# Optimization experiments

Hardware: AMD Instinct MI355X
Metric: run time of the kernel (lower is better)

The kernel has to match this reference:

```python
import jax, jax.numpy as jnp
import numpy as np

H, W, C = 128, 128, 100
N_OBJ = 3
PAD_VAL = 1e20  # WRONG_LABEL_PADDING-style padding used by local_pairwise_distances2


def setup_inputs() -> dict:
    key = jax.random.key(0)
    k1, k2, k3 = jax.random.split(key, 3)
    return {
        "prev_frame_embedding": jax.random.normal(k1, (H, W, C), dtype=jnp.float32),
        "query_embedding": jax.random.normal(k2, (H, W, C), dtype=jnp.float32),
        "prev_frame_labels": jax.random.randint(k3, (H, W, 1), 0, N_OBJ),
        "gt_ids": jnp.arange(N_OBJ),
        "max_distance": 15,
    }


def _local_nn_features(query_embedding, prev_frame_embedding, prev_frame_labels, gt_ids, max_distance):
    h, w, c = query_embedding.shape
    k = 2 * max_distance + 1  # static python int -> static shapes
    n_obj = gt_ids.shape[0]

    # masks: [h, w, n_obj] -- labels are [h, w, 1], broadcast against gt_ids
    masks = prev_frame_labels == gt_ids[None, None, :]

    # pad reference embedding with a huge value (matches torch F.pad value=1e20),
    # pad masks with False (matches torch zero padding)
    y_pad = jnp.pad(prev_frame_embedding,
                    ((max_distance, max_distance), (max_distance, max_distance), (0, 0)),
                    constant_values=PAD_VAL)
    m_pad = jnp.pad(masks,
                    ((max_distance, max_distance), (max_distance, max_distance), (0, 0)))

    # offsets in the same order as the torch nested loops (y_start outer, x_start inner)
    offs = jnp.stack(jnp.meshgrid(jnp.arange(k), jnp.arange(k), indexing="ij"), -1).reshape(-1, 2)

    x = query_embedding

    def per_offset(off):
        y_sl = jax.lax.dynamic_slice(y_pad, (off[0], off[1], 0), (h, w, c))
        m_sl = jax.lax.dynamic_slice(m_pad, (off[0], off[1], 0), (h, w, n_obj))
        diff = x - y_sl
        d = jnp.sum(diff * diff, axis=-1)  # [h, w]
        return d, m_sl

    # sequential map over the k*k window offsets keeps peak memory small
    d, offset_masks = jax.lax.map(per_offset, offs)  # [k2,h,w], [k2,h,w,n_obj]
    d = jnp.transpose(d, (1, 2, 0))                   # [h, w, k2]
    offset_masks = jnp.transpose(offset_masks, (1, 2, 0, 3))  # [h, w, k2, n_obj]

    # mask out wrong-object / out-of-frame offsets with distance 1.0 (torch pad=ones_like)
    d_masked = jnp.where(offset_masks, d[..., None], jnp.float32(1.0))
    dists = jnp.min(d_masked, axis=2)  # [h, w, n_obj]
    return dists.reshape(1, h, w, n_obj, 1)


def reference(prev_frame_embedding, query_embedding, prev_frame_labels, gt_ids, max_distance):
    return _local_nn_features(query_embedding, prev_frame_embedding,
                              prev_frame_labels, gt_ids, max_distance)
```

## Files before the change

### kernel.cpp

```cpp
#include <hip/hip_runtime.h>
#include <cstdint>


#define HW   128
#define NC   100
#define MD   15
#define NOBJ 3
#define PIX  (HW * HW)
#define NOUT (PIX * NOBJ)
#define PEN_NM (1 << 22)
#define CSENT  (1 << 28)
#define IINIT  (1 << 30)

typedef __attribute__((ext_vector_type(4))) int intx4;

__device__ inline intx4 quant_pack16(const float* v) {
    signed char b[16];
#pragma unroll
    for (int j = 0; j < 16; ++j) {
        int qi = __float2int_rn(v[j] * 32.f);
        b[j] = (signed char)max(-127, min(127, qi));
    }
    intx4 r;
#pragma unroll
    for (int w = 0; w < 4; ++w)
        r[w] = (b[4*w] & 255) | ((b[4*w+1] & 255) << 8) |
               ((b[4*w+2] & 255) << 16) | ((b[4*w+3] & 255) << 24);
    return r;
}

__global__ __launch_bounds__(256) void vos_prep(
    const float* __restrict__ P, const float* __restrict__ Q,
    const int* __restrict__ labels,
    signed char* __restrict__ Pq, signed char* __restrict__ Qa,
    int2* __restrict__ yl, float* __restrict__ x2)
{
    const int lane = threadIdx.x & 63;
    const int wid  = blockIdx.x * 4 + (threadIdx.x >> 6);

    if (wid < 2048) {
        const int pix = wid * 8 + (lane >> 3);
        const int col = pix & 127;
        const int c = lane & 7;
        const float* sp = P + (size_t)pix * NC;
        const int k0 = c * 16;
        float v[16];
#pragma unroll
        for (int c4 = 0; c4 < 4; ++c4) {
            float4 a = {0.f,0.f,0.f,0.f};
            if (k0 + c4 * 4 + 4 <= NC) a = *(const float4*)(sp + k0 + c4 * 4);
            v[c4*4+0]=a.x; v[c4*4+1]=a.y; v[c4*4+2]=a.z; v[c4*4+3]=a.w;
        }
        *(intx4*)(Pq + (size_t)pix * 128 + ((c ^ (col & 7)) << 4)) = quant_pack16(v);
        float part = 0.f;
#pragma unroll
        for (int j = 0; j < 16; ++j) part = fmaf(v[j], v[j], part);
        part += __shfl_xor(part, 1); part += __shfl_xor(part, 2); part += __shfl_xor(part, 4);
        if ((lane & 7) == 0)
            yl[pix] = make_int2(__float2int_rn(part * 512.f), labels[pix]);
    } else if (wid < 4096) {
        const int w2 = wid - 2048;
        const int row = w2 >> 4, rem = w2 & 15;
        const int tile = rem >> 1, kh = rem & 1;
        const int m = lane & 15, quad = lane >> 4;
        const int pix = row * HW + tile * 16 + m;
        const float* sp = Q + (size_t)pix * NC;
        const int k0 = kh * 64 + quad * 16;
        float v[16];
#pragma unroll
        for (int c4 = 0; c4 < 4; ++c4) {
            float4 a = {0.f,0.f,0.f,0.f};
            if (k0 + c4 * 4 + 4 <= NC) a = *(const float4*)(sp + k0 + c4 * 4);
            v[c4*4+0]=a.x; v[c4*4+1]=a.y; v[c4*4+2]=a.z; v[c4*4+3]=a.w;
        }
        *(intx4*)(Qa + ((size_t)((row*8 + tile)*2 + kh))*1024 + lane*16) = quant_pack16(v);
    } else {
        const int w3 = wid - 4096;
        const int pix = w3 * 8 + (lane >> 3);
        const int lp = lane & 7;
        const float* sp = Q + (size_t)pix * NC;
        float part = 0.f;
#pragma unroll
        for (int cc = 0; cc < 4; ++cc) {
            int k = lp * 16 + cc * 4;
            if (k <= 96) {
                float4 t = *(const float4*)(sp + k);
                part = fmaf(t.x,t.x,part); part = fmaf(t.y,t.y,part);
                part = fmaf(t.z,t.z,part); part = fmaf(t.w,t.w,part);
            }
        }
        part += __shfl_xor(part, 1); part += __shfl_xor(part, 2); part += __shfl_xor(part, 4);
        if (lp == 0) x2[pix] = part;
    }
}

__device__ inline void stage_row(const signed char* __restrict__ Pq,
                                 signed char* dst, int r, int wv, int lane) {
    const signed char* src = Pq + (size_t)r * 16384 + wv * 4096;
    signed char* d = dst + wv * 4096;
#pragma unroll
    for (int it = 0; it < 4; ++it)
        __builtin_amdgcn_global_load_lds(
            (const __attribute__((address_space(1))) unsigned int*)(src + it * 1024 + lane * 16),
            (__attribute__((address_space(3))) unsigned int*)(d + it * 1024), 16, 0, 0);
}

__global__ __launch_bounds__(256, 2) void vos_band(
    const signed char* __restrict__ Pq, const signed char* __restrict__ Qa,
    const int2* __restrict__ yl, const int* __restrict__ gt,
    float* __restrict__ part)
{
    __shared__ signed char Bs[2][2][16384];
    __shared__ int2 yl_s[4 * 128];

    const int tid  = threadIdx.x;
    const int lane = tid & 63;
    const int wv   = tid >> 6;
    const int quad = lane >> 4;
    const int n    = lane & 15;
    const int j0w  = wv * 32;

    const int b      = blockIdx.x;
    const int xcd    = b & 7;
    const int wi     = b >> 3;
    const int stripe = xcd * 8 + (wi & 7);
    const int ck     = wi >> 3;
    const int i0     = stripe * 2;
    const int rbase  = i0 - MD + ck * 4;
    const int rlo    = max(rbase, 0);
    const int rhi    = min(rbase + 4, HW);
    const int np     = (rhi > rlo) ? ((rhi - rlo + 1) >> 1) : 0;

    const int g0 = gt[0], g1 = gt[1], g2 = gt[2];

    if (np > 0) {
        stage_row(Pq, &Bs[0][0][0], rlo, wv, lane);
        if (rlo + 1 < rhi) stage_row(Pq, &Bs[0][1][0], rlo + 1, wv, lane);
    }

    for (int t = tid; t < 4 * 128; t += 256) {
        int rr = t >> 7, c = t & 127, r = rbase + rr;
        if ((unsigned)r < (unsigned)HW) yl_s[t] = yl[r * HW + c];
    }

    intx4 Af[2][2][2];
#pragma unroll
    for (int uc = 0; uc < 2; ++uc)
#pragma unroll
    for (int ur = 0; ur < 2; ++ur) {
        const signed char* bse = Qa + (size_t)((i0 + ur) * 8 + wv * 2 + uc) * 2048;
#pragma unroll
        for (int kh = 0; kh < 2; ++kh)
            Af[uc][ur][kh] = *(const intx4*)(bse + kh * 1024 + lane * 16);
    }

    bool bgt[4], blt[4];
#pragma unroll
    for (int reg = 0; reg < 4; ++reg) {
        int m = quad * 4 + reg;
        bgt[reg] = n > m;
        blt[reg] = n < m;
    }

    int mm[2][2][4][NOBJ];
#pragma unroll
    for (int uc = 0; uc < 2; ++uc)
#pragma unroll
    for (int ur = 0; ur < 2; ++ur)
#pragma unroll
    for (int reg = 0; reg < 4; ++reg) {
        mm[uc][ur][reg][0] = IINIT; mm[uc][ur][reg][1] = IINIT; mm[uc][ur][reg][2] = IINIT;
    }

    __syncthreads();

    for (int pi = 0; pi < np; ++pi) {
        const int ra = rlo + 2 * pi;
        const int rb = ra + 1;
        if (pi + 1 < np) {
            const int r2 = ra + 2;
            stage_row(Pq, &Bs[(pi + 1) & 1][0][0], r2, wv, lane);
            if (r2 + 1 < rhi) stage_row(Pq, &Bs[(pi + 1) & 1][1][0], r2 + 1, wv, lane);
        }

        const signed char* BA = &Bs[pi & 1][0][0];
        const signed char* BB = &Bs[pi & 1][1][0];
        const bool hasB = rb < rhi;
        bool rvA[2], rvB[2];
        rvA[0] = (unsigned)(ra - i0 + MD)     <= 2u * MD;
        rvA[1] = (unsigned)(ra - i0 - 1 + MD) <= 2u * MD;
        rvB[0] = hasB && ((unsigned)(rb - i0 + MD)     <= 2u * MD);
        rvB[1] = hasB && ((unsigned)(rb - i0 - 1 + MD) <= 2u * MD);
        const int rrA = (ra - rbase) * 128;
        const int rrB = (min(rb, rhi - 1) - rbase) * 128;

#pragma unroll
        for (int t = 0; t < 4; ++t) {
            const int base = j0w + 16 * (t - 1);
            if (base < 0 || base >= HW) continue;

            const int pcol = base + n;
            int2 ylA = yl_s[rrA + pcol];
            int2 ylB = yl_s[rrB + pcol];
            int pA0 = (ylA.y == g0) ? ylA.x : PEN_NM;
            int pA1 = (ylA.y == g1) ? ylA.x : PEN_NM;
            int pA2 = (ylA.y == g2) ? ylA.x : PEN_NM;
            int pB0 = (ylB.y == g0) ? ylB.x : PEN_NM;
            int pB1 = (ylB.y == g1) ? ylB.x : PEN_NM;
            int pB2 = (ylB.y == g2) ? ylB.x : PEN_NM;

            intx4 CA[2][2], CB[2][2];
#pragma unroll
            for (int uc = 0; uc < 2; ++uc)
#pragma unroll
            for (int ur = 0; ur < 2; ++ur) {
                CA[uc][ur] = (intx4){0,0,0,0};
                CB[uc][ur] = (intx4){0,0,0,0};
            }

#pragma unroll
            for (int kh = 0; kh < 2; ++kh) {
                const int off = pcol * 128 + (((kh * 4 + quad) ^ (pcol & 7)) << 4);
                intx4 bvA = *(const intx4*)(BA + off);
                intx4 bvB = *(const intx4*)(BB + off);
#pragma unroll
                for (int uc = 0; uc < 2; ++uc) {
                    if (uc == 0 && t == 3) continue;
                    if (uc == 1 && t == 0) continue;
#pragma unroll
                    for (int ur = 0; ur < 2; ++ur) {
                        CA[uc][ur] = __builtin_amdgcn_mfma_i32_16x16x64_i8(Af[uc][ur][kh], bvA, CA[uc][ur], 0, 0, 0);
                        CB[uc][ur] = __builtin_amdgcn_mfma_i32_16x16x64_i8(Af[uc][ur][kh], bvB, CB[uc][ur], 0, 0, 0);
                    }
                }
            }

#pragma unroll
            for (int uc = 0; uc < 2; ++uc) {
                if (uc == 0 && t == 3) continue;
                if (uc == 1 && t == 0) continue;
                const int du = t - 1 - uc;
#pragma unroll
                for (int ur = 0; ur < 2; ++ur) {
#pragma unroll
                    for (int reg = 0; reg < 4; ++reg) {
                        bool tri = (du == 0) | (du == -1 ? bgt[reg] : blt[reg]);
                        bool okA = rvA[ur] & tri;
                        bool okB = rvB[ur] & tri;
                        int cA = okA ? CA[uc][ur][reg] : -CSENT;
                        int cB = okB ? CB[uc][ur][reg] : -CSENT;
                        mm[uc][ur][reg][0] = min(min(mm[uc][ur][reg][0], pA0 - cA), pB0 - cB);
                        mm[uc][ur][reg][1] = min(min(mm[uc][ur][reg][1], pA1 - cA), pB1 - cB);
                        mm[uc][ur][reg][2] = min(min(mm[uc][ur][reg][2], pA2 - cA), pB2 - cB);
                    }
                }
            }
        }
        __syncthreads();
    }

#pragma unroll
    for (int s = 1; s < 16; s <<= 1) {
#pragma unroll
        for (int uc = 0; uc < 2; ++uc)
#pragma unroll
        for (int ur = 0; ur < 2; ++ur)
#pragma unroll
        for (int reg = 0; reg < 4; ++reg)
#pragma unroll
        for (int o = 0; o < NOBJ; ++o)
            mm[uc][ur][reg][o] = min(mm[uc][ur][reg][o], __shfl_xor(mm[uc][ur][reg][o], s));
    }

    float* ps = (float*)&Bs[0][0][0];
    if (n == 0) {
#pragma unroll
        for (int uc = 0; uc < 2; ++uc)
#pragma unroll
        for (int ur = 0; ur < 2; ++ur)
#pragma unroll
        for (int reg = 0; reg < 4; ++reg) {
            const int qcol = j0w + 16 * uc + quad * 4 + reg;
#pragma unroll
            for (int o = 0; o < NOBJ; ++o)
                ps[(ur * 128 + qcol) * 3 + o] = (float)mm[uc][ur][reg][o];
        }
    }
    __syncthreads();
    if (tid < 192) {
        float4 v = *(const float4*)(ps + tid * 4);
        *(float4*)(part + (size_t)ck * NOUT + i0 * 384 + tid * 4) = v;
    }
}

__global__ __launch_bounds__(256) void vos_combine(
    const float* __restrict__ part, const float* __restrict__ x2,
    float* __restrict__ out)
{
    const int t = blockIdx.x * 256 + threadIdx.x;
    float v = part[t];
#pragma unroll
    for (int ck = 1; ck < 8; ++ck) v = fminf(v, part[ck * NOUT + t]);
    v = v * (1.f / 512.f) + x2[t / 3];
    out[t] = fminf(fmaxf(v, 0.f), 1.0f);
}

extern "C" void kernel_launch(void* const* d_in, const int* in_sizes, int n_in,
                              void* d_out, int out_size, void* d_ws, size_t ws_size,
                              hipStream_t stream) {
    const float* P      = (const float*)d_in[0];
    const float* Q      = (const float*)d_in[1];
    const int*   labels = (const int*)d_in[2];
    const int*   gt     = (const int*)d_in[3];

    int2*  yl = (int2*)d_ws;
    float* x2 = (float*)(yl + PIX);
    signed char* Pq = (signed char*)(x2 + PIX);
    signed char* Qa = Pq + (size_t)PIX * 128;
    float* part = (float*)(Qa + (size_t)PIX * 128);
    float* out = (float*)d_out;

    vos_prep<<<1536, 256, 0, stream>>>(P, Q, labels, Pq, Qa, yl, x2);
    vos_band<<<512, 256, 0, stream>>>(Pq, Qa, yl, gt, part);
    vos_combine<<<NOUT / 256, 256, 0, stream>>>(part, x2, out);
}
```

Baseline: 87.26 us.

## Fuse combine into band kernel via last-block atomic counter; merge Q prep passes

Removes the separate combine launch. Each band block now bumps a per-stripe atomic counter, and the last of the 8 chunk blocks for a stripe does the min-reduction, scaling and clamping straight into the output. In the prep kernel, query quantization and the squared-norm computation are merged so each wave reads Q once, which halves the prep grid. This adds atomics and threadfences to the band kernel's tail, and it relies on the prep kernel zeroing the counters before the band kernel starts.

```diff
diff --git a/kernel.cpp b/kernel.cpp
--- a/kernel.cpp
+++ b/kernel.cpp
@@ -33,10 +33,12 @@
     const float* __restrict__ P, const float* __restrict__ Q,
     const int* __restrict__ labels,
     signed char* __restrict__ Pq, signed char* __restrict__ Qa,
-    int2* __restrict__ yl, float* __restrict__ x2)
+    int2* __restrict__ yl, float* __restrict__ x2, int* __restrict__ cnt)
 {
     const int lane = threadIdx.x & 63;
     const int wid  = blockIdx.x * 4 + (threadIdx.x >> 6);
+
+    if (blockIdx.x == 0 && threadIdx.x < 64) cnt[threadIdx.x] = 0;
 
     if (wid < 2048) {
         const int pix = wid * 8 + (lane >> 3);
@@ -58,39 +60,29 @@
         part += __shfl_xor(part, 1); part += __shfl_xor(part, 2); part += __shfl_xor(part, 4);
         if ((lane & 7) == 0)
             yl[pix] = make_int2(__float2int_rn(part * 512.f), labels[pix]);
-    } else if (wid < 4096) {
+    } else if (wid < 3072) {
         const int w2 = wid - 2048;
-        const int row = w2 >> 4, rem = w2 & 15;
-        const int tile = rem >> 1, kh = rem & 1;
+        const int row = w2 >> 3, tile = w2 & 7;
         const int m = lane & 15, quad = lane >> 4;
         const int pix = row * HW + tile * 16 + m;
         const float* sp = Q + (size_t)pix * NC;
-        const int k0 = kh * 64 + quad * 16;
-        float v[16];
-#pragma unroll
-        for (int c4 = 0; c4 < 4; ++c4) {
-            float4 a = {0.f,0.f,0.f,0.f};
-            if (k0 + c4 * 4 + 4 <= NC) a = *(const float4*)(sp + k0 + c4 * 4);
-            v[c4*4+0]=a.x; v[c4*4+1]=a.y; v[c4*4+2]=a.z; v[c4*4+3]=a.w;
-        }
-        *(intx4*)(Qa + ((size_t)((row*8 + tile)*2 + kh))*1024 + lane*16) = quant_pack16(v);
-    } else {
-        const int w3 = wid - 4096;
-        const int pix = w3 * 8 + (lane >> 3);
-        const int lp = lane & 7;
-        const float* sp = Q + (size_t)pix * NC;
-        float part = 0.f;
-#pragma unroll
-        for (int cc = 0; cc < 4; ++cc) {
-            int k = lp * 16 + cc * 4;
-            if (k <= 96) {
-                float4 t = *(const float4*)(sp + k);
-                part = fmaf(t.x,t.x,part); part = fmaf(t.y,t.y,part);
-                part = fmaf(t.z,t.z,part); part = fmaf(t.w,t.w,part);
+        float acc = 0.f;
+#pragma unroll
+        for (int kh = 0; kh < 2; ++kh) {
+            const int k0 = kh * 64 + quad * 16;
+            float v[16];
+#pragma unroll
+            for (int c4 = 0; c4 < 4; ++c4) {
+                float4 a = {0.f,0.f,0.f,0.f};
+                if (k0 + c4 * 4 + 4 <= NC) a = *(const float4*)(sp + k0 + c4 * 4);
+                v[c4*4+0]=a.x; v[c4*4+1]=a.y; v[c4*4+2]=a.z; v[c4*4+3]=a.w;
             }
-        }
-        part += __shfl_xor(part, 1); part += __shfl_xor(part, 2); part += __shfl_xor(part, 4);
-        if (lp == 0) x2[pix] = part;
+#pragma unroll
+            for (int j = 0; j < 16; ++j) acc = fmaf(v[j], v[j], acc);
+            *(intx4*)(Qa + ((size_t)((row*8 + tile)*2 + kh))*1024 + lane*16) = quant_pack16(v);
+        }
+        acc += __shfl_xor(acc, 16); acc += __shfl_xor(acc, 32);
+        if (quad == 0) x2[pix] = acc;
     }
 }
 
@@ -108,10 +100,12 @@
 __global__ __launch_bounds__(256, 2) void vos_band(
     const signed char* __restrict__ Pq, const signed char* __restrict__ Qa,
     const int2* __restrict__ yl, const int* __restrict__ gt,
-    float* __restrict__ part)
+    float* __restrict__ part, const float* __restrict__ x2,
+    float* __restrict__ out, int* __restrict__ cnt)
 {
     __shared__ signed char Bs[2][2][16384];
     __shared__ int2 yl_s[4 * 128];
+    __shared__ int last;
 
     const int tid  = threadIdx.x;
     const int lane = tid & 63;
@@ -291,18 +285,30 @@
         float4 v = *(const float4*)(ps + tid * 4);
         *(float4*)(part + (size_t)ck * NOUT + i0 * 384 + tid * 4) = v;
     }
-}
-
-__global__ __launch_bounds__(256) void vos_combine(
-    const float* __restrict__ part, const float* __restrict__ x2,
-    float* __restrict__ out)
-{
-    const int t = blockIdx.x * 256 + threadIdx.x;
-    float v = part[t];
-#pragma unroll
-    for (int ck = 1; ck < 8; ++ck) v = fminf(v, part[ck * NOUT + t]);
-    v = v * (1.f / 512.f) + x2[t / 3];
-    out[t] = fminf(fmaxf(v, 0.f), 1.0f);
+
+    __threadfence();
+    __syncthreads();
+    if (tid == 0) {
+        int old = atomicAdd(&cnt[stripe], 1);
+        last = (old == 7);
+    }
+    __syncthreads();
+    if (last) {
+        __threadfence();
+        const int pix = i0 * 128 + tid;
+        const float xv = x2[pix];
+        const float* pp = part + (size_t)i0 * 384 + tid * 3;
+        float v0 = pp[0], v1 = pp[1], v2 = pp[2];
+#pragma unroll
+        for (int c = 1; c < 8; ++c) {
+            const float* q = pp + (size_t)c * NOUT;
+            v0 = fminf(v0, q[0]); v1 = fminf(v1, q[1]); v2 = fminf(v2, q[2]);
+        }
+        float* op = out + (size_t)pix * 3;
+        op[0] = fminf(fmaxf(v0 * (1.f/512.f) + xv, 0.f), 1.0f);
+        op[1] = fminf(fmaxf(v1 * (1.f/512.f) + xv, 0.f), 1.0f);
+        op[2] = fminf(fmaxf(v2 * (1.f/512.f) + xv, 0.f), 1.0f);
+    }
 }
 
 extern "C" void kernel_launch(void* const* d_in, const int* in_sizes, int n_in,
@@ -318,9 +324,9 @@
     signed char* Pq = (signed char*)(x2 + PIX);
     signed char* Qa = Pq + (size_t)PIX * 128;
     float* part = (float*)(Qa + (size_t)PIX * 128);
+    int*   cnt  = (int*)(part + 8 * NOUT);
     float* out = (float*)d_out;
 
-    vos_prep<<<1536, 256, 0, stream>>>(P, Q, labels, Pq, Qa, yl, x2);
-    vos_band<<<512, 256, 0, stream>>>(Pq, Qa, yl, gt, part);
-    vos_combine<<<NOUT / 256, 256, 0, stream>>>(part, x2, out);
-}
+    vos_prep<<<768, 256, 0, stream>>>(P, Q, labels, Pq, Qa, yl, x2, cnt);
+    vos_band<<<512, 256, 0, stream>>>(Pq, Qa, yl, gt, part, x2, out, cnt);
+}
```

New measurement: 123.4 us. 41.4% more time.
